# Kernel optimization log

Hardware: AMD Instinct MI355X
Metric: run time of the kernel (lower is better)

Reference implementation:

```python
import jax, jax.numpy as jnp
import numpy as np

EPS = 1e-5
NUM_GROUPS = 8

def group_norm(x, gamma, beta):
    B, C, D, H, W = x.shape
    g = NUM_GROUPS
    xg = x.reshape(B, g, C // g, D, H, W)
    mu = xg.mean(axis=(2, 3, 4, 5), keepdims=True)
    var = xg.var(axis=(2, 3, 4, 5), keepdims=True)
    xn = ((xg - mu) / jnp.sqrt(var + EPS)).reshape(B, C, D, H, W)
    return xn * gamma[None, :, None, None, None] + beta[None, :, None, None, None]

def setup_inputs() -> dict:
    key = jax.random.key(0)
    ks = jax.random.split(key, 7)
    B, C, D, H, W = 4, 256, 16, 16, 16
    x = jax.random.normal(ks[0], (B, C, D, H, W), dtype=jnp.float32)
    gn_gamma = jnp.ones((C,), dtype=jnp.float32)
    gn_beta = jnp.zeros((C,), dtype=jnp.float32)
    # 1x1x1 conv weights stored as [out, in] matrices
    s = 1.0 / np.sqrt(C)
    qkv_w = jax.random.uniform(ks[1], (3 * C, C), minval=-s, maxval=s, dtype=jnp.float32)
    qkv_b = jax.random.uniform(ks[2], (3 * C,), minval=-s, maxval=s, dtype=jnp.float32)
    proj_w = jax.random.uniform(ks[3], (C, C), minval=-s, maxval=s, dtype=jnp.float32)
    proj_b = jax.random.uniform(ks[4], (C,), minval=-s, maxval=s, dtype=jnp.float32)
    return {"x": x, "gn_gamma": gn_gamma, "gn_beta": gn_beta,
            "qkv_w": qkv_w, "qkv_b": qkv_b, "proj_w": proj_w, "proj_b": proj_b}

def reference(x, gn_gamma, gn_beta, qkv_w, qkv_b, proj_w, proj_b):
    B, C, D, H, W = x.shape
    N = D * H * W
    h = group_norm(x, gn_gamma, gn_beta)
    hf = h.reshape(B, C, N)  # (B, C, N)
    # 1x1x1 conv == channel matmul
    qkv = jnp.einsum('oc,bcn->bon', qkv_w, hf) + qkv_b[None, :, None]  # (B, 3C, N)
    q, k, v = jnp.split(qkv, 3, axis=1)  # each (B, C, N)
    q = q.transpose(0, 2, 1)  # (B, N, C)
    k = k.transpose(0, 2, 1)
    v = v.transpose(0, 2, 1)
    scale = C ** (-0.5)
    attn = jnp.einsum('bnc,bmc->bnm', q, k) * scale  # (B, N, N)
    attn = jax.nn.softmax(attn, axis=-1)
    o = jnp.einsum('bnm,bmc->bnc', attn, v)  # (B, N, C)
    o = o.transpose(0, 2, 1)  # (B, C, N)
    o = jnp.einsum('oc,bcn->bon', proj_w, o) + proj_b[None, :, None]
    return x + o.reshape(B, C, D, H, W)
```

## Files before the change

kernel.cpp:

```cpp
#include <hip/hip_runtime.h>
#include <hip/hip_bf16.h>

typedef unsigned short u16;
typedef unsigned int u32;
typedef __attribute__((ext_vector_type(8))) short short8;
typedef __attribute__((ext_vector_type(4))) short short4v;
typedef __attribute__((ext_vector_type(4))) float f32x4;

static __device__ __forceinline__ u16 f2bf(float f) {
    union { float f; unsigned u; } a; a.f = f;
    unsigned u = a.u;
    u += 0x7FFFu + ((u >> 16) & 1u);
    return (u16)(u >> 16);
}
static __device__ __forceinline__ float bf2f(u16 h) {
    union { u32 u; float f; } a; a.u = ((u32)h) << 16; return a.f;
}
static __device__ __forceinline__ void gload16(const u16* g, u16* l) {
    __builtin_amdgcn_global_load_lds((const __attribute__((address_space(1))) u32*)(const void*)g,
                                     (__attribute__((address_space(3))) u32*)(void*)l, 16, 0, 0);
}

__global__ __launch_bounds__(256) void k_gnstats(const float* __restrict__ x, float* __restrict__ stats) {
    const int bg = blockIdx.x;
    const float* p = x + (size_t)bg * (32 * 4096);
    const int t = threadIdx.x;
    float s = 0.f, ss = 0.f;
    for (int i = t * 4; i < 32 * 4096; i += 256 * 4) {
        float4 v = *reinterpret_cast<const float4*>(p + i);
        s  += v.x + v.y + v.z + v.w;
        ss += v.x * v.x + v.y * v.y + v.z * v.z + v.w * v.w;
    }
    for (int off = 1; off < 64; off <<= 1) { s += __shfl_xor(s, off); ss += __shfl_xor(ss, off); }
    __shared__ float ls[4], lss[4];
    if ((t & 63) == 0) { ls[t >> 6] = s; lss[t >> 6] = ss; }
    __syncthreads();
    if (t == 0) {
        float S  = ls[0] + ls[1] + ls[2] + ls[3];
        float SS = lss[0] + lss[1] + lss[2] + lss[3];
        const float inv = 1.f / (32.f * 4096.f);
        float mu  = S * inv;
        float var = SS * inv - mu * mu;
        stats[bg * 2]     = mu;
        stats[bg * 2 + 1] = rsqrtf(var + 1e-5f);
    }
}

__global__ __launch_bounds__(256) void k_wconv(const float* __restrict__ qw, const float* __restrict__ pw,
                                               u16* __restrict__ q2, u16* __restrict__ p2) {
    const int i = (blockIdx.x * 256 + threadIdx.x) * 4;
    const float* src; u16* dst;
    if (i < 196608) { src = qw + i; dst = q2 + i; }
    else            { src = pw + (i - 196608); dst = p2 + (i - 196608); }
    float4 v = *reinterpret_cast<const float4*>(src);
    u16 o[4] = { f2bf(v.x), f2bf(v.y), f2bf(v.z), f2bf(v.w) };
    *reinterpret_cast<uint2*>(dst) = *reinterpret_cast<uint2*>(o);
}

__global__ __launch_bounds__(256) void k_norm(const float* __restrict__ x, const float* __restrict__ gamma,
                                              const float* __restrict__ beta, const float* __restrict__ stats,
                                              u16* __restrict__ H) {
    __shared__ u16 T[64][72];
    const int b = blockIdx.z, c0 = blockIdx.y * 64, n0 = blockIdx.x * 64;
    const int t = threadIdx.x;
    const int cl = t >> 2, nb = (t & 3) * 16;
    const int c = c0 + cl;
    const float mu = stats[(b * 8 + (c >> 5)) * 2];
    const float rstd = stats[(b * 8 + (c >> 5)) * 2 + 1];
    const float ga = gamma[c] * rstd, be = beta[c] - mu * ga;
    const float* xp = &x[((size_t)b * 256 + c) * 4096 + n0 + nb];
#pragma unroll
    for (int j = 0; j < 16; j += 4) {
        float4 v = *reinterpret_cast<const float4*>(xp + j);
        T[cl][nb + j + 0] = f2bf(v.x * ga + be);
        T[cl][nb + j + 1] = f2bf(v.y * ga + be);
        T[cl][nb + j + 2] = f2bf(v.z * ga + be);
        T[cl][nb + j + 3] = f2bf(v.w * ga + be);
    }
    __syncthreads();
    const int nl = t >> 2, cb = (t & 3) * 16;
    short8 s0, s1;
#pragma unroll
    for (int j = 0; j < 8; ++j) { s0[j] = (short)T[cb + j][nl]; s1[j] = (short)T[cb + 8 + j][nl]; }
    u16* dst = &H[((size_t)b * 4096 + n0 + nl) * 256 + c0 + cb];
    *reinterpret_cast<short8*>(dst)     = s0;
    *reinterpret_cast<short8*>(dst + 8) = s1;
}

__global__ __launch_bounds__(256) void k_qkv(const u16* __restrict__ H, const u16* __restrict__ W2,
                                             const float* __restrict__ qkv_b,
                                             u16* __restrict__ Q, u16* __restrict__ K, u16* __restrict__ V) {
    __shared__ u16 T[9216];
    const int b = blockIdx.z, o0 = blockIdx.x * 64, nb0 = blockIdx.y * 128;
    const int t = threadIdx.x, w = t >> 6, l = t & 63, lr = l & 15, lg = l >> 4;
    const size_t bN = (size_t)b * 4096;
    f32x4 acc[2][4];
#pragma unroll
    for (int m = 0; m < 2; ++m)
#pragma unroll
        for (int nf = 0; nf < 4; ++nf) acc[m][nf] = f32x4{0.f, 0.f, 0.f, 0.f};
    const u16* A0 = &H[(bN + nb0 + w * 32 + lr) * 256];
    const u16* A1 = A0 + 16 * 256;
#pragma unroll
    for (int cc = 0; cc < 8; ++cc) {
        short8 af0 = *reinterpret_cast<const short8*>(A0 + cc * 32 + lg * 8);
        short8 af1 = *reinterpret_cast<const short8*>(A1 + cc * 32 + lg * 8);
#pragma unroll
        for (int nf = 0; nf < 4; ++nf) {
            short8 bf = *reinterpret_cast<const short8*>(&W2[(size_t)(o0 + nf * 16 + lr) * 256 + cc * 32 + lg * 8]);
            acc[0][nf] = __builtin_amdgcn_mfma_f32_16x16x32_bf16(af0, bf, acc[0][nf], 0, 0, 0);
            acc[1][nf] = __builtin_amdgcn_mfma_f32_16x16x32_bf16(af1, bf, acc[1][nf], 0, 0, 0);
        }
    }
    const int og = o0 >> 8;
    const float scal = (og == 0) ? 0.0625f * 1.44269504f : 1.0f;
    float bias[4];
#pragma unroll
    for (int nf = 0; nf < 4; ++nf) bias[nf] = qkv_b[o0 + nf * 16 + lr];
    if (og < 2) {
#pragma unroll
        for (int m = 0; m < 2; ++m)
#pragma unroll
            for (int nf = 0; nf < 4; ++nf)
#pragma unroll
                for (int i = 0; i < 4; ++i)
                    T[(w * 32 + m * 16 + lg * 4 + i) * 72 + nf * 16 + lr] = f2bf((acc[m][nf][i] + bias[nf]) * scal);
        __syncthreads();
        const int rl = t >> 1, half = (t & 1) * 32;
        u16* dst = (og == 0 ? Q : K) + (bN + nb0 + rl) * 256 + (o0 & 255) + half;
#pragma unroll
        for (int j = 0; j < 4; ++j)
            *reinterpret_cast<short8*>(dst + j * 8) = *reinterpret_cast<short8*>(&T[rl * 72 + half + j * 8]);
    } else {
#pragma unroll
        for (int m = 0; m < 2; ++m)
#pragma unroll
            for (int nf = 0; nf < 4; ++nf)
#pragma unroll
                for (int i = 0; i < 4; ++i)
                    T[(nf * 16 + lr) * 144 + w * 32 + m * 16 + lg * 4 + i] = f2bf(acc[m][nf][i] + bias[nf]);
        __syncthreads();
        const int ol = t >> 2, nbl = (t & 3) * 32;
        const int s_ = (ol >> 1) & 7;
        u16* dst = V + ((size_t)b * 256 + (o0 - 512) + ol) * 4096 + nb0 + nbl;
#pragma unroll
        for (int j = 0; j < 4; ++j) {
            short8 vv = *reinterpret_cast<short8*>(&T[ol * 144 + nbl + j * 8]);
            short8 ov;
            if (s_ & 1) ov = short8{vv[4], vv[5], vv[6], vv[7], vv[0], vv[1], vv[2], vv[3]};
            else        ov = vv;
            *reinterpret_cast<short8*>(dst + (((2 * j) ^ (s_ & 6)) * 4)) = ov;
        }
    }
}

__global__ __launch_bounds__(256, 2) void k_flash(const u16* __restrict__ Qw, const u16* __restrict__ Kw,
                                                  const u16* __restrict__ Vw, u16* __restrict__ Opart,
                                                  float* __restrict__ ml) {
    __shared__ u16 Ks[2][8192];
    __shared__ u16 Vs[2][8192];
    const int b = blockIdx.z, sp = blockIdx.y;
    const int tid = threadIdx.x;
    const int w = tid >> 6, l = tid & 63;
    const int lr = l & 15, lg = l >> 4;
    const int qbase = blockIdx.x * 128 + w * 32;
    const int kb0 = sp * 1024;
    const size_t bN = (size_t)b * 4096;

    const u16* srcK = Kw + (bN + kb0 + (tid >> 5)) * 256 + (((tid & 31) * 8) ^ ((tid >> 5) * 8));
    const u16* srcV = Vw + ((size_t)b * 256 + (tid >> 2)) * 4096 + kb0 + (tid & 3) * 8;

#define STAGE(d, toff) { \
        const u16* sk_ = srcK + (size_t)(toff) * 8192; \
        const u16* sv_ = srcV + (toff) * 32; \
        gload16(sk_,              Ks[d] + tid * 8); \
        gload16(sk_ + 2048,       Ks[d] + 2048 + tid * 8); \
        gload16(sk_ + 4096,       Ks[d] + 4096 + tid * 8); \
        gload16(sk_ + 6144,       Ks[d] + 6144 + tid * 8); \
        gload16(sv_,              Vs[d] + tid * 8); \
        gload16(sv_ + 64 * 4096,  Vs[d] + 2048 + tid * 8); \
        gload16(sv_ + 128 * 4096, Vs[d] + 4096 + tid * 8); \
        gload16(sv_ + 192 * 4096, Vs[d] + 6144 + tid * 8); }

    const int c6 = (lr >> 2) & 1;
    int kofs[2];
#pragma unroll
    for (int n = 0; n < 2; ++n) kofs[n] = (n * 16 + lr) * 256 + ((lg * 8) ^ ((lr & 3) * 8));
    const int vslotA = ((lg ^ (lr >> 1)) * 4);
    const int vslotB = vslotA ^ 16;

    short8 qf[2][8];
#pragma unroll
    for (int m = 0; m < 2; ++m)
#pragma unroll
        for (int cc = 0; cc < 8; ++cc)
            qf[m][cc] = *reinterpret_cast<const short8*>(&Qw[(bN + qbase + m * 16 + lr) * 256 + cc * 32 + lg * 8]);

    f32x4 Oa[2][16];
    float mr[2], lsum[2];
#pragma unroll
    for (int m = 0; m < 2; ++m) {
#pragma unroll
        for (int cs = 0; cs < 16; ++cs) Oa[m][cs] = f32x4{0.f, 0.f, 0.f, 0.f};
        mr[m] = -1e30f; lsum[m] = 0.f;
    }

    STAGE(0, 0);
    for (int kt = 0; kt < 32; ++kt) {
        const int d = kt & 1;
        if (kt < 31) {
            STAGE(d ^ 1, kt + 1);
            asm volatile("s_waitcnt vmcnt(8)" ::: "memory");
        } else {
            asm volatile("s_waitcnt vmcnt(0)" ::: "memory");
        }
        __builtin_amdgcn_sched_barrier(0);
        __builtin_amdgcn_s_barrier();

        f32x4 sc[2][2];
#pragma unroll
        for (int m = 0; m < 2; ++m)
#pragma unroll
            for (int n = 0; n < 2; ++n) sc[m][n] = f32x4{0.f, 0.f, 0.f, 0.f};
        __builtin_amdgcn_s_setprio(1);
#pragma unroll
        for (int cc = 0; cc < 8; ++cc) {
            const int cb = ((cc ^ c6) << 5);
            short8 kf0 = *reinterpret_cast<const short8*>(&Ks[d][kofs[0] + cb]);
            short8 kf1 = *reinterpret_cast<const short8*>(&Ks[d][kofs[1] + cb]);
            sc[0][0] = __builtin_amdgcn_mfma_f32_16x16x32_bf16(kf0, qf[0][cc], sc[0][0], 0, 0, 0);
            sc[0][1] = __builtin_amdgcn_mfma_f32_16x16x32_bf16(kf1, qf[0][cc], sc[0][1], 0, 0, 0);
            sc[1][0] = __builtin_amdgcn_mfma_f32_16x16x32_bf16(kf0, qf[1][cc], sc[1][0], 0, 0, 0);
            sc[1][1] = __builtin_amdgcn_mfma_f32_16x16x32_bf16(kf1, qf[1][cc], sc[1][1], 0, 0, 0);
        }
        __builtin_amdgcn_s_setprio(0);

        float tmax[2];
        bool need = false;
#pragma unroll
        for (int m = 0; m < 2; ++m) {
            float tm = fmaxf(fmaxf(fmaxf(sc[m][0][0], sc[m][0][1]), fmaxf(sc[m][0][2], sc[m][0][3])),
                             fmaxf(fmaxf(sc[m][1][0], sc[m][1][1]), fmaxf(sc[m][1][2], sc[m][1][3])));
            tm = fmaxf(tm, __shfl_xor(tm, 16));
            tm = fmaxf(tm, __shfl_xor(tm, 32));
            tmax[m] = tm;
            need = need || (tm > mr[m] + 8.f);
        }
        if (__any(need)) {
            float av[2][4];
#pragma unroll
            for (int m = 0; m < 2; ++m) {
                float mn = fmaxf(mr[m], tmax[m]);
                float al = exp2f(mr[m] - mn);
                mr[m] = mn;
                lsum[m] *= al;
#pragma unroll
                for (int i = 0; i < 4; ++i) av[m][i] = __shfl(al, lg * 4 + i);
            }
#pragma unroll
            for (int m = 0; m < 2; ++m)
#pragma unroll
                for (int cs = 0; cs < 16; ++cs)
#pragma unroll
                    for (int i = 0; i < 4; ++i) Oa[m][cs][i] *= av[m][i];
        }
        short8 pf[2];
#pragma unroll
        for (int m = 0; m < 2; ++m) {
            float la = 0.f;
#pragma unroll
            for (int n = 0; n < 2; ++n)
#pragma unroll
                for (int i = 0; i < 4; ++i) {
                    float p = exp2f(sc[m][n][i] - mr[m]);
                    la += p;
                    pf[m][n * 4 + i] = (short)f2bf(p);
                }
            lsum[m] += la;
        }
        __builtin_amdgcn_s_setprio(1);
#pragma unroll
        for (int cs = 0; cs < 16; ++cs) {
            const int base = (cs * 16 + lr) * 32;
            short4v lo = *reinterpret_cast<const short4v*>(&Vs[d][base + vslotA]);
            short4v hi = *reinterpret_cast<const short4v*>(&Vs[d][base + vslotB]);
            short8 vf = __builtin_shufflevector(lo, hi, 0, 1, 2, 3, 4, 5, 6, 7);
            Oa[0][cs] = __builtin_amdgcn_mfma_f32_16x16x32_bf16(pf[0], vf, Oa[0][cs], 0, 0, 0);
            Oa[1][cs] = __builtin_amdgcn_mfma_f32_16x16x32_bf16(pf[1], vf, Oa[1][cs], 0, 0, 0);
        }
        __builtin_amdgcn_s_setprio(0);
        __builtin_amdgcn_s_barrier();
    }
#undef STAGE

    float lt[2];
#pragma unroll
    for (int m = 0; m < 2; ++m) {
        float ts = lsum[m];
        ts += __shfl_xor(ts, 16);
        ts += __shfl_xor(ts, 32);
        lt[m] = ts;
    }
    const size_t obase = ((size_t)(b * 4 + sp) * 4096 + qbase);
#pragma unroll
    for (int m = 0; m < 2; ++m)
#pragma unroll
        for (int cs = 0; cs < 16; ++cs)
#pragma unroll
            for (int i = 0; i < 4; ++i)
                Opart[(obase + m * 16 + lg * 4 + i) * 256 + cs * 16 + lr] = f2bf(Oa[m][cs][i]);
    if (lg == 0) {
#pragma unroll
        for (int m = 0; m < 2; ++m) {
            size_t r = obase + m * 16 + lr;
            ml[r * 2]     = mr[m];
            ml[r * 2 + 1] = lt[m];
        }
    }
}

__global__ __launch_bounds__(256) void k_comb(const u16* __restrict__ Opart, const float* __restrict__ ml,
                                              u16* __restrict__ Obf) {
    const int row = blockIdx.x * 8 + (threadIdx.x >> 5);
    const int b = row >> 12;
    const int c0 = (threadIdx.x & 31) * 8;
    const size_t rbase = (size_t)b * 4 * 4096 + (row & 4095);
    float ms[4], lsv[4];
#pragma unroll
    for (int s = 0; s < 4; ++s) {
        ms[s]  = ml[(rbase + (size_t)s * 4096) * 2];
        lsv[s] = ml[(rbase + (size_t)s * 4096) * 2 + 1];
    }
    float M = fmaxf(fmaxf(ms[0], ms[1]), fmaxf(ms[2], ms[3]));
    float W[4], L = 0.f;
#pragma unroll
    for (int s = 0; s < 4; ++s) { W[s] = exp2f(ms[s] - M); L += W[s] * lsv[s]; }
    const float inv = 1.f / L;
    float o[8] = {};
#pragma unroll
    for (int s = 0; s < 4; ++s) {
        short8 v = *reinterpret_cast<const short8*>(&Opart[(rbase + (size_t)s * 4096) * 256 + c0]);
#pragma unroll
        for (int j = 0; j < 8; ++j) o[j] += W[s] * bf2f((u16)v[j]);
    }
    short8 r;
#pragma unroll
    for (int j = 0; j < 8; ++j) r[j] = (short)f2bf(o[j] * inv);
    *reinterpret_cast<short8*>(&Obf[(size_t)row * 256 + c0]) = r;
}

__global__ __launch_bounds__(256) void k_proj(const u16* __restrict__ O, const u16* __restrict__ Wp,
                                              const float* __restrict__ proj_b, const float* __restrict__ x,
                                              float* __restrict__ out) {
    __shared__ float T[64][132];
    const int b = blockIdx.z, c0 = blockIdx.x * 64, nb0 = blockIdx.y * 128;
    const int t = threadIdx.x, w = t >> 6, l = t & 63, lr = l & 15, lg = l >> 4;
    const size_t bN = (size_t)b * 4096;
    f32x4 acc[2][4];
#pragma unroll
    for (int m = 0; m < 2; ++m)
#pragma unroll
        for (int nf = 0; nf < 4; ++nf) acc[m][nf] = f32x4{0.f, 0.f, 0.f, 0.f};
    const u16* A0 = &O[(bN + nb0 + w * 32 + lr) * 256];
    const u16* A1 = A0 + 16 * 256;
#pragma unroll
    for (int cc = 0; cc < 8; ++cc) {
        short8 af0 = *reinterpret_cast<const short8*>(A0 + cc * 32 + lg * 8);
        short8 af1 = *reinterpret_cast<const short8*>(A1 + cc * 32 + lg * 8);
#pragma unroll
        for (int nf = 0; nf < 4; ++nf) {
            short8 bf = *reinterpret_cast<const short8*>(&Wp[(size_t)(c0 + nf * 16 + lr) * 256 + cc * 32 + lg * 8]);
            acc[0][nf] = __builtin_amdgcn_mfma_f32_16x16x32_bf16(af0, bf, acc[0][nf], 0, 0, 0);
            acc[1][nf] = __builtin_amdgcn_mfma_f32_16x16x32_bf16(af1, bf, acc[1][nf], 0, 0, 0);
        }
    }
#pragma unroll
    for (int m = 0; m < 2; ++m)
#pragma unroll
        for (int nf = 0; nf < 4; ++nf)
#pragma unroll
            for (int i = 0; i < 4; ++i)
                T[nf * 16 + lr][w * 32 + m * 16 + lg * 4 + i] = acc[m][nf][i];
    __syncthreads();
    const int cl = t >> 2, nbl = (t & 3) * 32;
    const float pb = proj_b[c0 + cl];
    const size_t base = ((size_t)b * 256 + c0 + cl) * 4096 + nb0 + nbl;
#pragma unroll
    for (int j = 0; j < 32; j += 4) {
        float4 xv = *reinterpret_cast<const float4*>(&x[base + j]);
        float4 r;
        r.x = xv.x + T[cl][nbl + j + 0] + pb;
        r.y = xv.y + T[cl][nbl + j + 1] + pb;
        r.z = xv.z + T[cl][nbl + j + 2] + pb;
        r.w = xv.w + T[cl][nbl + j + 3] + pb;
        *reinterpret_cast<float4*>(&out[base + j]) = r;
    }
}

extern "C" void kernel_launch(void* const* d_in, const int* in_sizes, int n_in,
                              void* d_out, int out_size, void* d_ws, size_t ws_size,
                              hipStream_t stream) {
    const float* x      = (const float*)d_in[0];
    const float* gngam  = (const float*)d_in[1];
    const float* gnbeta = (const float*)d_in[2];
    const float* qkv_w  = (const float*)d_in[3];
    const float* qkv_b  = (const float*)d_in[4];
    const float* proj_w = (const float*)d_in[5];
    const float* proj_b = (const float*)d_in[6];
    float* out = (float*)d_out;

    char* wsb = (char*)d_ws;
    float* stats = (float*)wsb;
    u16* Hbf   = (u16*)(wsb + 1024);
    u16* Qws   = Hbf + 4194304;
    u16* Kws   = Qws + 4194304;
    u16* Vws   = Kws + 4194304;
    u16* W2q   = Vws + 4194304;
    u16* W2p   = W2q + 196608;
    u16* Opart = W2p + 65536;
    float* ml  = (float*)(Opart + 16777216);
    u16* Obf   = (u16*)(ml + 131072);

    k_gnstats<<<32, 256, 0, stream>>>(x, stats);
    k_wconv<<<256, 256, 0, stream>>>(qkv_w, proj_w, W2q, W2p);
    k_norm<<<dim3(64, 4, 4), 256, 0, stream>>>(x, gngam, gnbeta, stats, Hbf);
    k_qkv<<<dim3(12, 32, 4), 256, 0, stream>>>(Hbf, W2q, qkv_b, Qws, Kws, Vws);
    k_flash<<<dim3(32, 4, 4), 256, 0, stream>>>(Qws, Kws, Vws, Opart, ml);
    k_comb<<<2048, 256, 0, stream>>>(Opart, ml, Obf);
    k_proj<<<dim3(4, 32, 4), 256, 0, stream>>>(Obf, W2p, proj_b, x, out);
}
```

Before: 201.0 us.

## Halve flash query tile per wave, single-buffer K, raise occupancy

The flash kernel now gives each wave 16 query rows instead of 32, which halves the accumulator registers, and launches twice as many blocks. Occupancy rises from 2 to 3 blocks per CU. K is single-buffered and its next tile is staged after QK^T finishes, while V stays double-buffered. P is converted to bf16 with a packed conversion instruction. In exchange, each K/V tile loaded from global memory is reused across fewer queries, and the K load is less overlapped because of the full vmcnt(0) wait and the extra barrier.

```diff
diff --git a/kernel.cpp b/kernel.cpp
--- a/kernel.cpp
+++ b/kernel.cpp
@@ -15,6 +15,9 @@
 }
 static __device__ __forceinline__ float bf2f(u16 h) {
     union { u32 u; float f; } a; a.u = ((u32)h) << 16; return a.f;
+}
+static __device__ __forceinline__ u32 cvtpk(float lo, float hi) {
+    u32 r; asm("v_cvt_pk_bf16_f32 %0, %1, %2" : "=v"(r) : "v"(lo), "v"(hi)); return r;
 }
 static __device__ __forceinline__ void gload16(const u16* g, u16* l) {
     __builtin_amdgcn_global_load_lds((const __attribute__((address_space(1))) u32*)(const void*)g,
@@ -154,29 +157,28 @@
     }
 }
 
-__global__ __launch_bounds__(256, 2) void k_flash(const u16* __restrict__ Qw, const u16* __restrict__ Kw,
+__global__ __launch_bounds__(256, 3) void k_flash(const u16* __restrict__ Qw, const u16* __restrict__ Kw,
                                                   const u16* __restrict__ Vw, u16* __restrict__ Opart,
                                                   float* __restrict__ ml) {
-    __shared__ u16 Ks[2][8192];
+    __shared__ u16 Ks[8192];
     __shared__ u16 Vs[2][8192];
     const int b = blockIdx.z, sp = blockIdx.y;
     const int tid = threadIdx.x;
     const int w = tid >> 6, l = tid & 63;
     const int lr = l & 15, lg = l >> 4;
-    const int qbase = blockIdx.x * 128 + w * 32;
+    const int qbase = blockIdx.x * 64 + w * 16;
     const int kb0 = sp * 1024;
     const size_t bN = (size_t)b * 4096;
 
     const u16* srcK = Kw + (bN + kb0 + (tid >> 5)) * 256 + (((tid & 31) * 8) ^ ((tid >> 5) * 8));
     const u16* srcV = Vw + ((size_t)b * 256 + (tid >> 2)) * 4096 + kb0 + (tid & 3) * 8;
 
-#define STAGE(d, toff) { \
-        const u16* sk_ = srcK + (size_t)(toff) * 8192; \
-        const u16* sv_ = srcV + (toff) * 32; \
-        gload16(sk_,              Ks[d] + tid * 8); \
-        gload16(sk_ + 2048,       Ks[d] + 2048 + tid * 8); \
-        gload16(sk_ + 4096,       Ks[d] + 4096 + tid * 8); \
-        gload16(sk_ + 6144,       Ks[d] + 6144 + tid * 8); \
+#define STAGE_K(toff) { const u16* sk_ = srcK + (size_t)(toff) * 8192; \
+        gload16(sk_,        Ks + tid * 8); \
+        gload16(sk_ + 2048, Ks + 2048 + tid * 8); \
+        gload16(sk_ + 4096, Ks + 4096 + tid * 8); \
+        gload16(sk_ + 6144, Ks + 6144 + tid * 8); }
+#define STAGE_V(d, toff) { const u16* sv_ = srcV + (toff) * 32; \
         gload16(sv_,              Vs[d] + tid * 8); \
         gload16(sv_ + 64 * 4096,  Vs[d] + 2048 + tid * 8); \
         gload16(sv_ + 128 * 4096, Vs[d] + 4096 + tid * 8); \
@@ -189,133 +191,101 @@
     const int vslotA = ((lg ^ (lr >> 1)) * 4);
     const int vslotB = vslotA ^ 16;
 
-    short8 qf[2][8];
-#pragma unroll
-    for (int m = 0; m < 2; ++m)
-#pragma unroll
-        for (int cc = 0; cc < 8; ++cc)
-            qf[m][cc] = *reinterpret_cast<const short8*>(&Qw[(bN + qbase + m * 16 + lr) * 256 + cc * 32 + lg * 8]);
-
-    f32x4 Oa[2][16];
-    float mr[2], lsum[2];
-#pragma unroll
-    for (int m = 0; m < 2; ++m) {
-#pragma unroll
-        for (int cs = 0; cs < 16; ++cs) Oa[m][cs] = f32x4{0.f, 0.f, 0.f, 0.f};
-        mr[m] = -1e30f; lsum[m] = 0.f;
-    }
-
-    STAGE(0, 0);
+    short8 qf[8];
+#pragma unroll
+    for (int cc = 0; cc < 8; ++cc)
+        qf[cc] = *reinterpret_cast<const short8*>(&Qw[(bN + qbase + lr) * 256 + cc * 32 + lg * 8]);
+
+    f32x4 Oa[16];
+#pragma unroll
+    for (int cs = 0; cs < 16; ++cs) Oa[cs] = f32x4{0.f, 0.f, 0.f, 0.f};
+    float mr = -1e30f, lsum = 0.f;
+
+    STAGE_K(0);
+    STAGE_V(0, 0);
     for (int kt = 0; kt < 32; ++kt) {
-        const int d = kt & 1;
-        if (kt < 31) {
-            STAGE(d ^ 1, kt + 1);
-            asm volatile("s_waitcnt vmcnt(8)" ::: "memory");
-        } else {
-            asm volatile("s_waitcnt vmcnt(0)" ::: "memory");
-        }
+        const int dv = kt & 1;
+        asm volatile("s_waitcnt vmcnt(0)" ::: "memory");
         __builtin_amdgcn_sched_barrier(0);
         __builtin_amdgcn_s_barrier();
-
-        f32x4 sc[2][2];
-#pragma unroll
-        for (int m = 0; m < 2; ++m)
-#pragma unroll
-            for (int n = 0; n < 2; ++n) sc[m][n] = f32x4{0.f, 0.f, 0.f, 0.f};
+        if (kt < 31) STAGE_V(dv ^ 1, kt + 1);
+
+        f32x4 sc[2];
+        sc[0] = f32x4{0.f, 0.f, 0.f, 0.f};
+        sc[1] = f32x4{0.f, 0.f, 0.f, 0.f};
         __builtin_amdgcn_s_setprio(1);
 #pragma unroll
         for (int cc = 0; cc < 8; ++cc) {
             const int cb = ((cc ^ c6) << 5);
-            short8 kf0 = *reinterpret_cast<const short8*>(&Ks[d][kofs[0] + cb]);
-            short8 kf1 = *reinterpret_cast<const short8*>(&Ks[d][kofs[1] + cb]);
-            sc[0][0] = __builtin_amdgcn_mfma_f32_16x16x32_bf16(kf0, qf[0][cc], sc[0][0], 0, 0, 0);
-            sc[0][1] = __builtin_amdgcn_mfma_f32_16x16x32_bf16(kf1, qf[0][cc], sc[0][1], 0, 0, 0);
-            sc[1][0] = __builtin_amdgcn_mfma_f32_16x16x32_bf16(kf0, qf[1][cc], sc[1][0], 0, 0, 0);
-            sc[1][1] = __builtin_amdgcn_mfma_f32_16x16x32_bf16(kf1, qf[1][cc], sc[1][1], 0, 0, 0);
+            short8 kf0 = *reinterpret_cast<const short8*>(&Ks[kofs[0] + cb]);
+            short8 kf1 = *reinterpret_cast<const short8*>(&Ks[kofs[1] + cb]);
+            sc[0] = __builtin_amdgcn_mfma_f32_16x16x32_bf16(kf0, qf[cc], sc[0], 0, 0, 0);
+            sc[1] = __builtin_amdgcn_mfma_f32_16x16x32_bf16(kf1, qf[cc], sc[1], 0, 0, 0);
         }
         __builtin_amdgcn_s_setprio(0);
 
-        float tmax[2];
-        bool need = false;
-#pragma unroll
-        for (int m = 0; m < 2; ++m) {
-            float tm = fmaxf(fmaxf(fmaxf(sc[m][0][0], sc[m][0][1]), fmaxf(sc[m][0][2], sc[m][0][3])),
-                             fmaxf(fmaxf(sc[m][1][0], sc[m][1][1]), fmaxf(sc[m][1][2], sc[m][1][3])));
-            tm = fmaxf(tm, __shfl_xor(tm, 16));
-            tm = fmaxf(tm, __shfl_xor(tm, 32));
-            tmax[m] = tm;
-            need = need || (tm > mr[m] + 8.f);
-        }
-        if (__any(need)) {
-            float av[2][4];
-#pragma unroll
-            for (int m = 0; m < 2; ++m) {
-                float mn = fmaxf(mr[m], tmax[m]);
-                float al = exp2f(mr[m] - mn);
-                mr[m] = mn;
-                lsum[m] *= al;
-#pragma unroll
-                for (int i = 0; i < 4; ++i) av[m][i] = __shfl(al, lg * 4 + i);
+        float tm = fmaxf(fmaxf(fmaxf(sc[0][0], sc[0][1]), fmaxf(sc[0][2], sc[0][3])),
+                         fmaxf(fmaxf(sc[1][0], sc[1][1]), fmaxf(sc[1][2], sc[1][3])));
+        tm = fmaxf(tm, __shfl_xor(tm, 16));
+        tm = fmaxf(tm, __shfl_xor(tm, 32));
+        if (__any(tm > mr + 8.f)) {
+            float mn = fmaxf(mr, tm);
+            float al = exp2f(mr - mn);
+            mr = mn;
+            lsum *= al;
+            float av[4];
+#pragma unroll
+            for (int i = 0; i < 4; ++i) av[i] = __shfl(al, lg * 4 + i);
+#pragma unroll
+            for (int cs = 0; cs < 16; ++cs)
+#pragma unroll
+                for (int i = 0; i < 4; ++i) Oa[cs][i] *= av[i];
+        }
+        float pvv[8];
+        float la = 0.f;
+#pragma unroll
+        for (int n = 0; n < 2; ++n)
+#pragma unroll
+            for (int i = 0; i < 4; ++i) {
+                float p = exp2f(sc[n][i] - mr);
+                la += p;
+                pvv[n * 4 + i] = p;
             }
-#pragma unroll
-            for (int m = 0; m < 2; ++m)
-#pragma unroll
-                for (int cs = 0; cs < 16; ++cs)
-#pragma unroll
-                    for (int i = 0; i < 4; ++i) Oa[m][cs][i] *= av[m][i];
-        }
-        short8 pf[2];
-#pragma unroll
-        for (int m = 0; m < 2; ++m) {
-            float la = 0.f;
-#pragma unroll
-            for (int n = 0; n < 2; ++n)
-#pragma unroll
-                for (int i = 0; i < 4; ++i) {
-                    float p = exp2f(sc[m][n][i] - mr[m]);
-                    la += p;
-                    pf[m][n * 4 + i] = (short)f2bf(p);
-                }
-            lsum[m] += la;
-        }
+        lsum += la;
+        union { u32 uw[4]; short8 v; } pu;
+#pragma unroll
+        for (int j = 0; j < 4; ++j) pu.uw[j] = cvtpk(pvv[2 * j], pvv[2 * j + 1]);
+
+        __builtin_amdgcn_s_barrier();
+        if (kt < 31) STAGE_K(kt + 1);
+
         __builtin_amdgcn_s_setprio(1);
 #pragma unroll
         for (int cs = 0; cs < 16; ++cs) {
             const int base = (cs * 16 + lr) * 32;
-            short4v lo = *reinterpret_cast<const short4v*>(&Vs[d][base + vslotA]);
-            short4v hi = *reinterpret_cast<const short4v*>(&Vs[d][base + vslotB]);
+            short4v lo = *reinterpret_cast<const short4v*>(&Vs[dv][base + vslotA]);
+            short4v hi = *reinterpret_cast<const short4v*>(&Vs[dv][base + vslotB]);
             short8 vf = __builtin_shufflevector(lo, hi, 0, 1, 2, 3, 4, 5, 6, 7);
-            Oa[0][cs] = __builtin_amdgcn_mfma_f32_16x16x32_bf16(pf[0], vf, Oa[0][cs], 0, 0, 0);
-            Oa[1][cs] = __builtin_amdgcn_mfma_f32_16x16x32_bf16(pf[1], vf, Oa[1][cs], 0, 0, 0);
+            Oa[cs] = __builtin_amdgcn_mfma_f32_16x16x32_bf16(pu.v, vf, Oa[cs], 0, 0, 0);
         }
         __builtin_amdgcn_s_setprio(0);
-        __builtin_amdgcn_s_barrier();
-    }
-#undef STAGE
-
-    float lt[2];
-#pragma unroll
-    for (int m = 0; m < 2; ++m) {
-        float ts = lsum[m];
-        ts += __shfl_xor(ts, 16);
-        ts += __shfl_xor(ts, 32);
-        lt[m] = ts;
-    }
+    }
+#undef STAGE_K
+#undef STAGE_V
+
+    float ts = lsum;
+    ts += __shfl_xor(ts, 16);
+    ts += __shfl_xor(ts, 32);
     const size_t obase = ((size_t)(b * 4 + sp) * 4096 + qbase);
 #pragma unroll
-    for (int m = 0; m < 2; ++m)
-#pragma unroll
-        for (int cs = 0; cs < 16; ++cs)
-#pragma unroll
-            for (int i = 0; i < 4; ++i)
-                Opart[(obase + m * 16 + lg * 4 + i) * 256 + cs * 16 + lr] = f2bf(Oa[m][cs][i]);
+    for (int cs = 0; cs < 16; ++cs)
+#pragma unroll
+        for (int i = 0; i < 4; ++i)
+            Opart[(obase + lg * 4 + i) * 256 + cs * 16 + lr] = f2bf(Oa[cs][i]);
     if (lg == 0) {
-#pragma unroll
-        for (int m = 0; m < 2; ++m) {
-            size_t r = obase + m * 16 + lr;
-            ml[r * 2]     = mr[m];
-            ml[r * 2 + 1] = lt[m];
-        }
+        size_t r = obase + lr;
+        ml[r * 2]     = mr;
+        ml[r * 2 + 1] = ts;
     }
 }
 
@@ -425,7 +395,7 @@
     k_wconv<<<256, 256, 0, stream>>>(qkv_w, proj_w, W2q, W2p);
     k_norm<<<dim3(64, 4, 4), 256, 0, stream>>>(x, gngam, gnbeta, stats, Hbf);
     k_qkv<<<dim3(12, 32, 4), 256, 0, stream>>>(Hbf, W2q, qkv_b, Qws, Kws, Vws);
-    k_flash<<<dim3(32, 4, 4), 256, 0, stream>>>(Qws, Kws, Vws, Opart, ml);
+    k_flash<<<dim3(64, 4, 4), 256, 0, stream>>>(Qws, Kws, Vws, Opart, ml);
     k_comb<<<2048, 256, 0, stream>>>(Opart, ml, Obf);
     k_proj<<<dim3(4, 32, 4), 256, 0, stream>>>(Obf, W2p, proj_b, x, out);
 }
```

Result: slower. 225.8 us (+12.3%).

## Widen flash blocks to 8 waves with 64-key tiles and fuse prep kernels

Applied to the files above, without the earlier changes.

The flash-attention kernel now runs 512-thread blocks covering 256 queries. Each stage loads a 64-key K/V tile, processed as two 32-key sub-steps, so the tile is shared by twice as many waves. The loop uses one barrier per iteration and issues the next prefetch right after it, and P is packed to bf16 with the hardware v_cvt_pk_bf16_f32 instruction. The group-norm stats and weight-conversion kernels are merged into one launch to save a launch. In exchange, LDS per block doubles and only one block fits per CU, and waiting on vmcnt(0) at each iteration start may expose load latency.

```diff
diff --git a/kernel.cpp b/kernel.cpp
--- a/kernel.cpp
+++ b/kernel.cpp
@@ -16,15 +16,30 @@
 static __device__ __forceinline__ float bf2f(u16 h) {
     union { u32 u; float f; } a; a.u = ((u32)h) << 16; return a.f;
 }
+static __device__ __forceinline__ u32 cvtpk(float lo, float hi) {
+    u32 r; asm("v_cvt_pk_bf16_f32 %0, %1, %2" : "=v"(r) : "v"(lo), "v"(hi)); return r;
+}
 static __device__ __forceinline__ void gload16(const u16* g, u16* l) {
     __builtin_amdgcn_global_load_lds((const __attribute__((address_space(1))) u32*)(const void*)g,
                                      (__attribute__((address_space(3))) u32*)(void*)l, 16, 0, 0);
 }
 
-__global__ __launch_bounds__(256) void k_gnstats(const float* __restrict__ x, float* __restrict__ stats) {
+__global__ __launch_bounds__(256) void k_pre(const float* __restrict__ x, float* __restrict__ stats,
+                                             const float* __restrict__ qw, const float* __restrict__ pw,
+                                             u16* __restrict__ q2, u16* __restrict__ p2) {
+    const int t = threadIdx.x;
+    if (blockIdx.x >= 32) {
+        const int i = ((int)blockIdx.x - 32) * 1024 + t * 4;
+        const float* src; u16* dst;
+        if (i < 196608) { src = qw + i; dst = q2 + i; }
+        else            { src = pw + (i - 196608); dst = p2 + (i - 196608); }
+        float4 v = *reinterpret_cast<const float4*>(src);
+        u16 o[4] = { f2bf(v.x), f2bf(v.y), f2bf(v.z), f2bf(v.w) };
+        *reinterpret_cast<uint2*>(dst) = *reinterpret_cast<uint2*>(o);
+        return;
+    }
     const int bg = blockIdx.x;
     const float* p = x + (size_t)bg * (32 * 4096);
-    const int t = threadIdx.x;
     float s = 0.f, ss = 0.f;
     for (int i = t * 4; i < 32 * 4096; i += 256 * 4) {
         float4 v = *reinterpret_cast<const float4*>(p + i);
@@ -46,17 +61,6 @@
     }
 }
 
-__global__ __launch_bounds__(256) void k_wconv(const float* __restrict__ qw, const float* __restrict__ pw,
-                                               u16* __restrict__ q2, u16* __restrict__ p2) {
-    const int i = (blockIdx.x * 256 + threadIdx.x) * 4;
-    const float* src; u16* dst;
-    if (i < 196608) { src = qw + i; dst = q2 + i; }
-    else            { src = pw + (i - 196608); dst = p2 + (i - 196608); }
-    float4 v = *reinterpret_cast<const float4*>(src);
-    u16 o[4] = { f2bf(v.x), f2bf(v.y), f2bf(v.z), f2bf(v.w) };
-    *reinterpret_cast<uint2*>(dst) = *reinterpret_cast<uint2*>(o);
-}
-
 __global__ __launch_bounds__(256) void k_norm(const float* __restrict__ x, const float* __restrict__ gamma,
                                               const float* __restrict__ beta, const float* __restrict__ stats,
                                               u16* __restrict__ H) {
@@ -154,33 +158,33 @@
     }
 }
 
-__global__ __launch_bounds__(256, 2) void k_flash(const u16* __restrict__ Qw, const u16* __restrict__ Kw,
+__global__ __launch_bounds__(512, 1) void k_flash(const u16* __restrict__ Qw, const u16* __restrict__ Kw,
                                                   const u16* __restrict__ Vw, u16* __restrict__ Opart,
                                                   float* __restrict__ ml) {
-    __shared__ u16 Ks[2][8192];
-    __shared__ u16 Vs[2][8192];
+    __shared__ u16 Ks[2][16384];
+    __shared__ u16 Vs[2][16384];
     const int b = blockIdx.z, sp = blockIdx.y;
     const int tid = threadIdx.x;
     const int w = tid >> 6, l = tid & 63;
     const int lr = l & 15, lg = l >> 4;
-    const int qbase = blockIdx.x * 128 + w * 32;
+    const int qbase = blockIdx.x * 256 + w * 32;
     const int kb0 = sp * 1024;
     const size_t bN = (size_t)b * 4096;
 
-    const u16* srcK = Kw + (bN + kb0 + (tid >> 5)) * 256 + (((tid & 31) * 8) ^ ((tid >> 5) * 8));
-    const u16* srcV = Vw + ((size_t)b * 256 + (tid >> 2)) * 4096 + kb0 + (tid & 3) * 8;
+    const u16* srcK = Kw + (bN + kb0 + (tid >> 5)) * 256 + (((tid & 31) * 8) ^ (((tid >> 5) & 7) * 8));
+    const u16* srcV = Vw + ((size_t)b * 256 + (tid >> 3)) * 4096 + kb0 + (tid & 7) * 8;
 
 #define STAGE(d, toff) { \
-        const u16* sk_ = srcK + (size_t)(toff) * 8192; \
-        const u16* sv_ = srcV + (toff) * 32; \
-        gload16(sk_,              Ks[d] + tid * 8); \
-        gload16(sk_ + 2048,       Ks[d] + 2048 + tid * 8); \
-        gload16(sk_ + 4096,       Ks[d] + 4096 + tid * 8); \
-        gload16(sk_ + 6144,       Ks[d] + 6144 + tid * 8); \
-        gload16(sv_,              Vs[d] + tid * 8); \
-        gload16(sv_ + 64 * 4096,  Vs[d] + 2048 + tid * 8); \
-        gload16(sv_ + 128 * 4096, Vs[d] + 4096 + tid * 8); \
-        gload16(sv_ + 192 * 4096, Vs[d] + 6144 + tid * 8); }
+        const u16* sk_ = srcK + (size_t)(toff) * 16384; \
+        const u16* sv_ = srcV + (toff) * 64; \
+        gload16(sk_,               Ks[d] + tid * 8); \
+        gload16(sk_ + 16 * 256,    Ks[d] + 4096 + tid * 8); \
+        gload16(sk_ + 32 * 256,    Ks[d] + 8192 + tid * 8); \
+        gload16(sk_ + 48 * 256,    Ks[d] + 12288 + tid * 8); \
+        gload16(sv_,               Vs[d] + tid * 8); \
+        gload16(sv_ + 64 * 4096,   Vs[d] + 4096 + tid * 8); \
+        gload16(sv_ + 128 * 4096,  Vs[d] + 8192 + tid * 8); \
+        gload16(sv_ + 192 * 4096,  Vs[d] + 12288 + tid * 8); }
 
     const int c6 = (lr >> 2) & 1;
     int kofs[2];
@@ -206,90 +210,93 @@
     }
 
     STAGE(0, 0);
-    for (int kt = 0; kt < 32; ++kt) {
+    for (int kt = 0; kt < 16; ++kt) {
         const int d = kt & 1;
-        if (kt < 31) {
-            STAGE(d ^ 1, kt + 1);
-            asm volatile("s_waitcnt vmcnt(8)" ::: "memory");
-        } else {
-            asm volatile("s_waitcnt vmcnt(0)" ::: "memory");
-        }
+        asm volatile("s_waitcnt vmcnt(0)" ::: "memory");
         __builtin_amdgcn_sched_barrier(0);
         __builtin_amdgcn_s_barrier();
-
-        f32x4 sc[2][2];
-#pragma unroll
-        for (int m = 0; m < 2; ++m)
-#pragma unroll
-            for (int n = 0; n < 2; ++n) sc[m][n] = f32x4{0.f, 0.f, 0.f, 0.f};
-        __builtin_amdgcn_s_setprio(1);
-#pragma unroll
-        for (int cc = 0; cc < 8; ++cc) {
-            const int cb = ((cc ^ c6) << 5);
-            short8 kf0 = *reinterpret_cast<const short8*>(&Ks[d][kofs[0] + cb]);
-            short8 kf1 = *reinterpret_cast<const short8*>(&Ks[d][kofs[1] + cb]);
-            sc[0][0] = __builtin_amdgcn_mfma_f32_16x16x32_bf16(kf0, qf[0][cc], sc[0][0], 0, 0, 0);
-            sc[0][1] = __builtin_amdgcn_mfma_f32_16x16x32_bf16(kf1, qf[0][cc], sc[0][1], 0, 0, 0);
-            sc[1][0] = __builtin_amdgcn_mfma_f32_16x16x32_bf16(kf0, qf[1][cc], sc[1][0], 0, 0, 0);
-            sc[1][1] = __builtin_amdgcn_mfma_f32_16x16x32_bf16(kf1, qf[1][cc], sc[1][1], 0, 0, 0);
+        if (kt < 15) STAGE(d ^ 1, kt + 1);
+
+#pragma unroll
+        for (int st = 0; st < 2; ++st) {
+            const int kO = st * 8192;
+            const int vO = st * 32;
+            f32x4 sc[2][2];
+#pragma unroll
+            for (int m = 0; m < 2; ++m)
+#pragma unroll
+                for (int n = 0; n < 2; ++n) sc[m][n] = f32x4{0.f, 0.f, 0.f, 0.f};
+            __builtin_amdgcn_s_setprio(1);
+#pragma unroll
+            for (int cc = 0; cc < 8; ++cc) {
+                const int cb = ((cc ^ c6) << 5);
+                short8 kf0 = *reinterpret_cast<const short8*>(&Ks[d][kO + kofs[0] + cb]);
+                short8 kf1 = *reinterpret_cast<const short8*>(&Ks[d][kO + kofs[1] + cb]);
+                sc[0][0] = __builtin_amdgcn_mfma_f32_16x16x32_bf16(kf0, qf[0][cc], sc[0][0], 0, 0, 0);
+                sc[0][1] = __builtin_amdgcn_mfma_f32_16x16x32_bf16(kf1, qf[0][cc], sc[0][1], 0, 0, 0);
+                sc[1][0] = __builtin_amdgcn_mfma_f32_16x16x32_bf16(kf0, qf[1][cc], sc[1][0], 0, 0, 0);
+                sc[1][1] = __builtin_amdgcn_mfma_f32_16x16x32_bf16(kf1, qf[1][cc], sc[1][1], 0, 0, 0);
+            }
+            __builtin_amdgcn_s_setprio(0);
+
+            float tmax[2];
+            bool need = false;
+#pragma unroll
+            for (int m = 0; m < 2; ++m) {
+                float tm = fmaxf(fmaxf(fmaxf(sc[m][0][0], sc[m][0][1]), fmaxf(sc[m][0][2], sc[m][0][3])),
+                                 fmaxf(fmaxf(sc[m][1][0], sc[m][1][1]), fmaxf(sc[m][1][2], sc[m][1][3])));
+                tm = fmaxf(tm, __shfl_xor(tm, 16));
+                tm = fmaxf(tm, __shfl_xor(tm, 32));
+                tmax[m] = tm;
+                need = need || (tm > mr[m] + 8.f);
+            }
+            if (__any(need)) {
+                float av[2][4];
+#pragma unroll
+                for (int m = 0; m < 2; ++m) {
+                    float mn = fmaxf(mr[m], tmax[m]);
+                    float al = exp2f(mr[m] - mn);
+                    mr[m] = mn;
+                    lsum[m] *= al;
+#pragma unroll
+                    for (int i = 0; i < 4; ++i) av[m][i] = __shfl(al, lg * 4 + i);
+                }
+#pragma unroll
+                for (int m = 0; m < 2; ++m)
+#pragma unroll
+                    for (int cs = 0; cs < 16; ++cs)
+#pragma unroll
+                        for (int i = 0; i < 4; ++i) Oa[m][cs][i] *= av[m][i];
+            }
+            union { u32 uw[4]; short8 v; } pf[2];
+#pragma unroll
+            for (int m = 0; m < 2; ++m) {
+                float p[8];
+                float la = 0.f;
+#pragma unroll
+                for (int n = 0; n < 2; ++n)
+#pragma unroll
+                    for (int i = 0; i < 4; ++i) {
+                        float pv = exp2f(sc[m][n][i] - mr[m]);
+                        la += pv;
+                        p[n * 4 + i] = pv;
+                    }
+                lsum[m] += la;
+#pragma unroll
+                for (int j = 0; j < 4; ++j) pf[m].uw[j] = cvtpk(p[2 * j], p[2 * j + 1]);
+            }
+            __builtin_amdgcn_s_setprio(1);
+#pragma unroll
+            for (int cs = 0; cs < 16; ++cs) {
+                const int base = (cs * 16 + lr) * 64 + vO;
+                short4v lo = *reinterpret_cast<const short4v*>(&Vs[d][base + vslotA]);
+                short4v hi = *reinterpret_cast<const short4v*>(&Vs[d][base + vslotB]);
+                short8 vf = __builtin_shufflevector(lo, hi, 0, 1, 2, 3, 4, 5, 6, 7);
+                Oa[0][cs] = __builtin_amdgcn_mfma_f32_16x16x32_bf16(pf[0].v, vf, Oa[0][cs], 0, 0, 0);
+                Oa[1][cs] = __builtin_amdgcn_mfma_f32_16x16x32_bf16(pf[1].v, vf, Oa[1][cs], 0, 0, 0);
+            }
+            __builtin_amdgcn_s_setprio(0);
         }
-        __builtin_amdgcn_s_setprio(0);
-
-        float tmax[2];
-        bool need = false;
-#pragma unroll
-        for (int m = 0; m < 2; ++m) {
-            float tm = fmaxf(fmaxf(fmaxf(sc[m][0][0], sc[m][0][1]), fmaxf(sc[m][0][2], sc[m][0][3])),
-                             fmaxf(fmaxf(sc[m][1][0], sc[m][1][1]), fmaxf(sc[m][1][2], sc[m][1][3])));
-            tm = fmaxf(tm, __shfl_xor(tm, 16));
-            tm = fmaxf(tm, __shfl_xor(tm, 32));
-            tmax[m] = tm;
-            need = need || (tm > mr[m] + 8.f);
-        }
-        if (__any(need)) {
-            float av[2][4];
-#pragma unroll
-            for (int m = 0; m < 2; ++m) {
-                float mn = fmaxf(mr[m], tmax[m]);
-                float al = exp2f(mr[m] - mn);
-                mr[m] = mn;
-                lsum[m] *= al;
-#pragma unroll
-                for (int i = 0; i < 4; ++i) av[m][i] = __shfl(al, lg * 4 + i);
-            }
-#pragma unroll
-            for (int m = 0; m < 2; ++m)
-#pragma unroll
-                for (int cs = 0; cs < 16; ++cs)
-#pragma unroll
-                    for (int i = 0; i < 4; ++i) Oa[m][cs][i] *= av[m][i];
-        }
-        short8 pf[2];
-#pragma unroll
-        for (int m = 0; m < 2; ++m) {
-            float la = 0.f;
-#pragma unroll
-            for (int n = 0; n < 2; ++n)
-#pragma unroll
-                for (int i = 0; i < 4; ++i) {
-                    float p = exp2f(sc[m][n][i] - mr[m]);
-                    la += p;
-                    pf[m][n * 4 + i] = (short)f2bf(p);
-                }
-            lsum[m] += la;
-        }
-        __builtin_amdgcn_s_setprio(1);
-#pragma unroll
-        for (int cs = 0; cs < 16; ++cs) {
-            const int base = (cs * 16 + lr) * 32;
-            short4v lo = *reinterpret_cast<const short4v*>(&Vs[d][base + vslotA]);
-            short4v hi = *reinterpret_cast<const short4v*>(&Vs[d][base + vslotB]);
-            short8 vf = __builtin_shufflevector(lo, hi, 0, 1, 2, 3, 4, 5, 6, 7);
-            Oa[0][cs] = __builtin_amdgcn_mfma_f32_16x16x32_bf16(pf[0], vf, Oa[0][cs], 0, 0, 0);
-            Oa[1][cs] = __builtin_amdgcn_mfma_f32_16x16x32_bf16(pf[1], vf, Oa[1][cs], 0, 0, 0);
-        }
-        __builtin_amdgcn_s_setprio(0);
-        __builtin_amdgcn_s_barrier();
     }
 #undef STAGE
 
@@ -421,11 +428,10 @@
     float* ml  = (float*)(Opart + 16777216);
     u16* Obf   = (u16*)(ml + 131072);
 
-    k_gnstats<<<32, 256, 0, stream>>>(x, stats);
-    k_wconv<<<256, 256, 0, stream>>>(qkv_w, proj_w, W2q, W2p);
+    k_pre<<<288, 256, 0, stream>>>(x, stats, qkv_w, proj_w, W2q, W2p);
     k_norm<<<dim3(64, 4, 4), 256, 0, stream>>>(x, gngam, gnbeta, stats, Hbf);
     k_qkv<<<dim3(12, 32, 4), 256, 0, stream>>>(Hbf, W2q, qkv_b, Qws, Kws, Vws);
-    k_flash<<<dim3(32, 4, 4), 256, 0, stream>>>(Qws, Kws, Vws, Opart, ml);
+    k_flash<<<dim3(16, 4, 4), 512, 0, stream>>>(Qws, Kws, Vws, Opart, ml);
     k_comb<<<2048, 256, 0, stream>>>(Opart, ml, Obf);
     k_proj<<<dim3(4, 32, 4), 256, 0, stream>>>(Obf, W2p, proj_b, x, out);
 }
```

New measurement: 198.5 us. Within noise of the previous version (-1.2%).
